# Kernel tuning notes

Measured on AMD Instinct MI355X. Metric: run time of the kernel, lower is better.

Reference implementation:

```python
import jax, jax.numpy as jnp
import numpy as np

N = 50000      # nodes
E = 800000     # directed edges (avg degree 16)
F_IN = 128     # in_channels
HID = 256      # hidden_channels
OUT = 40       # out_channels (classes)


def setup_inputs() -> dict:
    key = jax.random.key(0)
    ks = jax.random.split(key, 6)
    x = jax.random.normal(ks[0], (N, F_IN), dtype=jnp.float32)
    edge_index = jax.random.randint(ks[1], (2, E), 0, N, dtype=jnp.int32)
    W1 = jax.random.normal(ks[2], (F_IN, HID), dtype=jnp.float32) * (1.0 / np.sqrt(F_IN))
    b1 = jnp.zeros((HID,), jnp.float32)
    W2 = jax.random.normal(ks[3], (HID, HID), dtype=jnp.float32) * (1.0 / np.sqrt(HID))
    b2 = jnp.zeros((HID,), jnp.float32)
    Wc = jax.random.normal(ks[4], (HID, OUT), dtype=jnp.float32) * (1.0 / np.sqrt(HID))
    bc = jnp.zeros((OUT,), jnp.float32)
    return {"x": x, "W1": W1, "b1": b1, "W2": W2, "b2": b2,
            "Wc": Wc, "bc": bc, "edge_index": edge_index}


def _gcn_conv(x, W, b, src, dst, norm):
    # PyG GCNConv: linear transform, then normalized sparse aggregation, then bias.
    h = x @ W                                    # [N, H]
    msg = h[src] * norm[:, None]                 # [E+N, H] gather + scale
    agg = jax.ops.segment_sum(msg, dst, num_segments=N)  # scatter-add
    return agg + b


def reference(x, W1, b1, W2, b2, Wc, bc, edge_index):
    # add self-loops (GCNConv default add_self_loops=True)
    loops = jnp.arange(N, dtype=edge_index.dtype)
    src = jnp.concatenate([edge_index[0], loops])
    dst = jnp.concatenate([edge_index[1], loops])
    # symmetric normalization D^-1/2 A D^-1/2 (degree counted at dst)
    deg = jax.ops.segment_sum(jnp.ones_like(dst, dtype=jnp.float32), dst,
                              num_segments=N)
    dinv = jax.lax.rsqrt(jnp.maximum(deg, 1.0))  # deg >= 1 due to self-loops
    norm = dinv[src] * dinv[dst]                 # [E+N]
    # layer 1 + ReLU (dropout is identity in eval mode)
    h = jax.nn.relu(_gcn_conv(x, W1, b1, src, dst, norm))
    # layer 2 + ReLU
    h = jax.nn.relu(_gcn_conv(h, W2, b2, src, dst, norm))
    # dense classifier
    return h @ Wc + bc  # [N, OUT]
```

## Files before the change

### kernel.cpp

```cpp
#include <hip/hip_runtime.h>

#define NNODES 50000
#define NEDGES 800000
#define F_IN   128
#define HID    256
#define NOUT   40
#define NBLK_SCAN ((NNODES + 255) / 256)
#define NBLK_CAST 6250
#define NBLK_DEG  2048
#define NBLK_PREP 432
#define EDGE_CHUNK 3125
#define NODES_PER_G 6250

typedef __attribute__((ext_vector_type(8))) _Float16 f16x8;
typedef __attribute__((ext_vector_type(4))) float f32x4;
typedef __attribute__((ext_vector_type(4))) unsigned short u16x4;
typedef __attribute__((ext_vector_type(8))) unsigned short u16x8;

__device__ __forceinline__ unsigned short f2h(float f) {
  return __builtin_bit_cast(unsigned short, (_Float16)f);
}
__device__ __forceinline__ float h2f(unsigned short u) {
  return (float)__builtin_bit_cast(_Float16, u);
}


__global__ __launch_bounds__(256) void k_pre(const float* __restrict__ X,
                                             unsigned short* __restrict__ Xh,
                                             const int* __restrict__ dst,
                                             int* __restrict__ count,
                                             const float* __restrict__ W1,
                                             const float* __restrict__ W2,
                                             const float* __restrict__ Wc,
                                             unsigned short* __restrict__ T1,
                                             unsigned short* __restrict__ T2,
                                             unsigned short* __restrict__ Tc) {
  int b = blockIdx.x, t = threadIdx.x;
  if (b < NBLK_CAST) {
    int i = b * 256 + t;
    float4 v = *reinterpret_cast<const float4*>(X + (size_t)i * 4);
    ushort4 o;
    o.x = f2h(v.x); o.y = f2h(v.y); o.z = f2h(v.z); o.w = f2h(v.w);
    *reinterpret_cast<ushort4*>(Xh + (size_t)i * 4) = o;
  } else if (b < NBLK_CAST + NBLK_DEG) {
    int db = b - NBLK_CAST;
    int g = b & 7;
    int chunk = db >> 3;
    int lo = g * NODES_PER_G, hi = lo + NODES_PER_G;
    int base = chunk * EDGE_CHUNK;
    for (int i = base + t; i < base + EDGE_CHUNK; i += 256) {
      int d = dst[i];
      if (d >= lo && d < hi) atomicAdd(&count[d], 1);
    }
  } else {
    int pb = b - NBLK_CAST - NBLK_DEG;
    if (pb < 128) {
      int idx = pb * 256 + t;
      int n = idx >> 7, k = idx & 127;
      T1[idx] = f2h(W1[(size_t)k * HID + n]);
    } else if (pb < 384) {
      int idx = (pb - 128) * 256 + t;
      int n = idx >> 8, k = idx & 255;
      T2[idx] = f2h(W2[(size_t)k * HID + n]);
    } else {
      int idx = (pb - 384) * 256 + t;
      int n = idx >> 8, k = idx & 255;
      float v = (n < NOUT) ? Wc[(size_t)k * NOUT + n] : 0.f;
      Tc[idx] = f2h(v);
    }
  }
}


__global__ __launch_bounds__(256) void k_scan1(const int* __restrict__ count,
                                               int* __restrict__ rowstart,
                                               int* __restrict__ bsum,
                                               float* __restrict__ dinv) {
  __shared__ int tmp[256];
  int t = threadIdx.x;
  int i = blockIdx.x * 256 + t;
  int v = (i < NNODES) ? count[i] : 0;
  if (i < NNODES) dinv[i] = rsqrtf((float)(v + 1));
  tmp[t] = v;
  __syncthreads();
  for (int off = 1; off < 256; off <<= 1) {
    int x = (t >= off) ? tmp[t - off] : 0;
    __syncthreads();
    tmp[t] += x;
    __syncthreads();
  }
  if (i < NNODES) rowstart[i] = tmp[t] - v;
  if (t == 255) bsum[blockIdx.x] = tmp[255];
}

__global__ __launch_bounds__(256) void k_scan2(const int* __restrict__ bsum,
                                               int* __restrict__ boff) {
  __shared__ int tmp[256];
  int t = threadIdx.x;
  int v = (t < NBLK_SCAN) ? bsum[t] : 0;
  tmp[t] = v;
  __syncthreads();
  for (int off = 1; off < 256; off <<= 1) {
    int x = (t >= off) ? tmp[t - off] : 0;
    __syncthreads();
    tmp[t] += x;
    __syncthreads();
  }
  if (t < NBLK_SCAN) boff[t] = tmp[t] - v;
}


__global__ __launch_bounds__(256) void k_scatter(const int* __restrict__ src,
                                                 const int* __restrict__ dst,
                                                 const int* __restrict__ rowstart,
                                                 const int* __restrict__ boff,
                                                 int* __restrict__ cursor,
                                                 int* __restrict__ csr) {
  int g = blockIdx.x & 7;
  int chunk = blockIdx.x >> 3;
  int lo = g * NODES_PER_G, hi = lo + NODES_PER_G;
  int base = chunk * EDGE_CHUNK;
  for (int i = base + threadIdx.x; i < base + EDGE_CHUNK; i += 256) {
    int d = dst[i];
    if (d >= lo && d < hi) {
      int p = rowstart[d] + boff[d >> 8] + atomicAdd(&cursor[d], 1);
      csr[p] = src[i];
    }
  }
}


__global__ __launch_bounds__(256) void k_agg1(const unsigned short* __restrict__ X,
                                              const int* __restrict__ rowstart,
                                              const int* __restrict__ boff,
                                              const int* __restrict__ csr,
                                              const float* __restrict__ dinv,
                                              uint2* __restrict__ Y) {
  int wave = threadIdx.x >> 6, lane = threadIdx.x & 63;
  int node = blockIdx.x * 4 + wave;
  if (node >= NNODES) return;
  int half = lane >> 5, l32 = lane & 31;
  float di = dinv[node];
  float a[4] = {0.f, 0.f, 0.f, 0.f};
  int e = rowstart[node] + boff[node >> 8];
  int end = (node + 1 < NNODES) ? rowstart[node + 1] + boff[(node + 1) >> 8] : NEDGES;
  for (; e + 8 <= end; e += 8) {
    int s0 = csr[e + 0 + half], s1 = csr[e + 2 + half];
    int s2 = csr[e + 4 + half], s3 = csr[e + 6 + half];
    float w0 = dinv[s0] * di, w1 = dinv[s1] * di;
    float w2 = dinv[s2] * di, w3 = dinv[s3] * di;
    u16x4 r0 = *reinterpret_cast<const u16x4*>(X + (size_t)s0 * F_IN + l32 * 4);
    u16x4 r1 = *reinterpret_cast<const u16x4*>(X + (size_t)s1 * F_IN + l32 * 4);
    u16x4 r2 = *reinterpret_cast<const u16x4*>(X + (size_t)s2 * F_IN + l32 * 4);
    u16x4 r3 = *reinterpret_cast<const u16x4*>(X + (size_t)s3 * F_IN + l32 * 4);
#pragma unroll
    for (int k = 0; k < 4; k++) {
      a[k] = fmaf(h2f(r0[k]), w0, a[k]);
      a[k] = fmaf(h2f(r1[k]), w1, a[k]);
      a[k] = fmaf(h2f(r2[k]), w2, a[k]);
      a[k] = fmaf(h2f(r3[k]), w3, a[k]);
    }
  }
  for (; e + 2 <= end; e += 2) {
    int s = csr[e + half];
    float w = dinv[s] * di;
    u16x4 r = *reinterpret_cast<const u16x4*>(X + (size_t)s * F_IN + l32 * 4);
#pragma unroll
    for (int k = 0; k < 4; k++) a[k] = fmaf(h2f(r[k]), w, a[k]);
  }
  if (e < end) {
    int s = csr[e];
    float w = half ? 0.f : dinv[s] * di;
    u16x4 r = *reinterpret_cast<const u16x4*>(X + (size_t)s * F_IN + l32 * 4);
#pragma unroll
    for (int k = 0; k < 4; k++) a[k] = fmaf(h2f(r[k]), w, a[k]);
  }
#pragma unroll
  for (int k = 0; k < 4; k++) a[k] += __shfl_xor(a[k], 32);
  if (half == 0) {
    u16x4 self = *reinterpret_cast<const u16x4*>(X + (size_t)node * F_IN + l32 * 4);
    float dd = di * di;
#pragma unroll
    for (int k = 0; k < 4; k++) a[k] = fmaf(h2f(self[k]), dd, a[k]);
    uint2 o;
    o.x = (unsigned)f2h(a[0]) | ((unsigned)f2h(a[1]) << 16);
    o.y = (unsigned)f2h(a[2]) | ((unsigned)f2h(a[3]) << 16);
    Y[(size_t)node * 32 + l32] = o;
  }
}


__global__ __launch_bounds__(256) void k_agg2(const unsigned short* __restrict__ H,
                                              const int* __restrict__ rowstart,
                                              const int* __restrict__ boff,
                                              const int* __restrict__ csr,
                                              const float* __restrict__ dinv,
                                              uint4* __restrict__ Y) {
  int wave = threadIdx.x >> 6, lane = threadIdx.x & 63;
  int node = blockIdx.x * 4 + wave;
  if (node >= NNODES) return;
  int half = lane >> 5, l32 = lane & 31;
  float di = dinv[node];
  float a[8] = {0.f, 0.f, 0.f, 0.f, 0.f, 0.f, 0.f, 0.f};
  int e = rowstart[node] + boff[node >> 8];
  int end = (node + 1 < NNODES) ? rowstart[node + 1] + boff[(node + 1) >> 8] : NEDGES;
  for (; e + 8 <= end; e += 8) {
    int s0 = csr[e + 0 + half], s1 = csr[e + 2 + half];
    int s2 = csr[e + 4 + half], s3 = csr[e + 6 + half];
    float w0 = dinv[s0] * di, w1 = dinv[s1] * di;
    float w2 = dinv[s2] * di, w3 = dinv[s3] * di;
    u16x8 r0 = *reinterpret_cast<const u16x8*>(H + (size_t)s0 * HID + l32 * 8);
    u16x8 r1 = *reinterpret_cast<const u16x8*>(H + (size_t)s1 * HID + l32 * 8);
    u16x8 r2 = *reinterpret_cast<const u16x8*>(H + (size_t)s2 * HID + l32 * 8);
    u16x8 r3 = *reinterpret_cast<const u16x8*>(H + (size_t)s3 * HID + l32 * 8);
#pragma unroll
    for (int k = 0; k < 8; k++) {
      a[k] = fmaf(h2f(r0[k]), w0, a[k]);
      a[k] = fmaf(h2f(r1[k]), w1, a[k]);
      a[k] = fmaf(h2f(r2[k]), w2, a[k]);
      a[k] = fmaf(h2f(r3[k]), w3, a[k]);
    }
  }
  for (; e + 2 <= end; e += 2) {
    int s = csr[e + half];
    float w = dinv[s] * di;
    u16x8 r = *reinterpret_cast<const u16x8*>(H + (size_t)s * HID + l32 * 8);
#pragma unroll
    for (int k = 0; k < 8; k++) a[k] = fmaf(h2f(r[k]), w, a[k]);
  }
  if (e < end) {
    int s = csr[e];
    float w = half ? 0.f : dinv[s] * di;
    u16x8 r = *reinterpret_cast<const u16x8*>(H + (size_t)s * HID + l32 * 8);
#pragma unroll
    for (int k = 0; k < 8; k++) a[k] = fmaf(h2f(r[k]), w, a[k]);
  }
#pragma unroll
  for (int k = 0; k < 8; k++) a[k] += __shfl_xor(a[k], 32);
  if (half == 0) {
    u16x8 self = *reinterpret_cast<const u16x8*>(H + (size_t)node * HID + l32 * 8);
    float dd = di * di;
#pragma unroll
    for (int k = 0; k < 8; k++) a[k] = fmaf(h2f(self[k]), dd, a[k]);
    uint4 o;
    o.x = (unsigned)f2h(a[0]) | ((unsigned)f2h(a[1]) << 16);
    o.y = (unsigned)f2h(a[2]) | ((unsigned)f2h(a[3]) << 16);
    o.z = (unsigned)f2h(a[4]) | ((unsigned)f2h(a[5]) << 16);
    o.w = (unsigned)f2h(a[6]) | ((unsigned)f2h(a[7]) << 16);
    Y[(size_t)node * 32 + l32] = o;
  }
}


template <int RELU, int OMODE>
__global__ __launch_bounds__(256) void k_mgemm(const unsigned short* __restrict__ Ag,
                                               const unsigned short* __restrict__ Btg,
                                               const float* __restrict__ bias,
                                               void* __restrict__ Cout,
                                               int M, int Nc, int K) {
  __shared__ unsigned short Ah[2][128 * 40];
  __shared__ unsigned short Bh[2][128 * 40];
  int tid = threadIdx.x;
  int lane = tid & 63, w = tid >> 6;
  int wr = w >> 1, wc = w & 1;
  int bm = blockIdx.x * 128, bn = blockIdx.y * 128;
  int l15 = lane & 15, kg = lane >> 4;
  int row0 = tid >> 2, kq0 = (tid & 3) * 8;
  int gm0 = bm + row0, gm1 = bm + row0 + 64;

  f32x4 zero = {0.f, 0.f, 0.f, 0.f};
  f32x4 acc[4][4];
#pragma unroll
  for (int i = 0; i < 4; i++)
#pragma unroll
    for (int j = 0; j < 4; j++) acc[i][j] = zero;

  uint4 ra0, ra1, rb0, rb1;
  const uint4 z4 = {0, 0, 0, 0};
#define LOADT(KT)                                                                    \
  {                                                                                  \
    ra0 = z4; ra1 = z4;                                                              \
    if (gm0 < M) ra0 = *reinterpret_cast<const uint4*>(Ag + (size_t)gm0 * K + (KT) + kq0); \
    if (gm1 < M) ra1 = *reinterpret_cast<const uint4*>(Ag + (size_t)gm1 * K + (KT) + kq0); \
    rb0 = *reinterpret_cast<const uint4*>(Btg + (size_t)(bn + row0) * K + (KT) + kq0);     \
    rb1 = *reinterpret_cast<const uint4*>(Btg + (size_t)(bn + row0 + 64) * K + (KT) + kq0);\
  }
#define STORET(B)                                                       \
  {                                                                     \
    *reinterpret_cast<uint4*>(&Ah[B][row0 * 40 + kq0]) = ra0;           \
    *reinterpret_cast<uint4*>(&Ah[B][(row0 + 64) * 40 + kq0]) = ra1;    \
    *reinterpret_cast<uint4*>(&Bh[B][row0 * 40 + kq0]) = rb0;           \
    *reinterpret_cast<uint4*>(&Bh[B][(row0 + 64) * 40 + kq0]) = rb1;    \
  }

  LOADT(0);
  STORET(0);
  __syncthreads();
  int nt = K >> 5, cur = 0;
  for (int t = 0; t < nt; t++) {
    bool pf = (t + 1 < nt);
    if (pf) LOADT((t + 1) << 5);
    f16x8 fa[4], fb[4];
#pragma unroll
    for (int f = 0; f < 4; f++) {
      fa[f] = *reinterpret_cast<const f16x8*>(&Ah[cur][(wr * 64 + f * 16 + l15) * 40 + kg * 8]);
      fb[f] = *reinterpret_cast<const f16x8*>(&Bh[cur][(wc * 64 + f * 16 + l15) * 40 + kg * 8]);
    }
#pragma unroll
    for (int i = 0; i < 4; i++)
#pragma unroll
      for (int j = 0; j < 4; j++)
        acc[i][j] = __builtin_amdgcn_mfma_f32_16x16x32_f16(fa[i], fb[j], acc[i][j], 0, 0, 0);
    if (pf) STORET(cur ^ 1);
    __syncthreads();
    cur ^= 1;
  }
#undef LOADT
#undef STORET

  int r0 = kg * 4;
#pragma unroll
  for (int i = 0; i < 4; i++) {
    int gmBase = bm + wr * 64 + i * 16 + r0;
#pragma unroll
    for (int r = 0; r < 4; r++) {
      int gm = gmBase + r;
      if (gm >= M) continue;
#pragma unroll
      for (int j = 0; j < 4; j++) {
        int gn = bn + wc * 64 + j * 16 + l15;
        if (gn >= Nc) continue;
        float v = acc[i][j][r] + bias[gn];
        if (RELU) v = fmaxf(v, 0.f);
        size_t o = (size_t)gm * Nc + gn;
        if (OMODE == 0) ((float*)Cout)[o] = v;
        else            ((unsigned short*)Cout)[o] = f2h(v);
      }
    }
  }
}


__global__ __launch_bounds__(256) void k_cls(const unsigned short* __restrict__ Ag,
                                             const unsigned short* __restrict__ Btg,
                                             const float* __restrict__ bias,
                                             float* __restrict__ C, int M) {
  __shared__ unsigned short As[256 * 40];
  __shared__ unsigned short Bs[48 * 40];
  int tid = threadIdx.x;
  int lane = tid & 63, w = tid >> 6;
  int l15 = lane & 15, kg = lane >> 4;
  int bm = blockIdx.x * 256;

  f32x4 zero = {0.f, 0.f, 0.f, 0.f};
  f32x4 acc[4][3];
#pragma unroll
  for (int i = 0; i < 4; i++)
#pragma unroll
    for (int j = 0; j < 3; j++) acc[i][j] = zero;

  for (int kt = 0; kt < HID; kt += 32) {
#pragma unroll
    for (int it = 0; it < 4; it++) {
      int c = tid + it * 256;
      int row = c >> 2, kq = (c & 3) * 8;
      int gm = bm + row;
      uint4 v = {0, 0, 0, 0};
      if (gm < M) v = *reinterpret_cast<const uint4*>(Ag + (size_t)gm * HID + kt + kq);
      *reinterpret_cast<uint4*>(&As[row * 40 + kq]) = v;
    }
    if (tid < 192) {
      int row = tid >> 2, kq = (tid & 3) * 8;
      *reinterpret_cast<uint4*>(&Bs[row * 40 + kq]) =
          *reinterpret_cast<const uint4*>(Btg + (size_t)row * HID + kt + kq);
    }
    __syncthreads();
    f16x8 fa[4], fb[3];
#pragma unroll
    for (int f = 0; f < 4; f++)
      fa[f] = *reinterpret_cast<const f16x8*>(&As[(w * 64 + f * 16 + l15) * 40 + kg * 8]);
#pragma unroll
    for (int j = 0; j < 3; j++)
      fb[j] = *reinterpret_cast<const f16x8*>(&Bs[(j * 16 + l15) * 40 + kg * 8]);
#pragma unroll
    for (int i = 0; i < 4; i++)
#pragma unroll
      for (int j = 0; j < 3; j++)
        acc[i][j] = __builtin_amdgcn_mfma_f32_16x16x32_f16(fa[i], fb[j], acc[i][j], 0, 0, 0);
    __syncthreads();
  }

  int r0 = kg * 4;
#pragma unroll
  for (int i = 0; i < 4; i++) {
    int gmBase = bm + w * 64 + i * 16 + r0;
#pragma unroll
    for (int r = 0; r < 4; r++) {
      int gm = gmBase + r;
      if (gm >= M) continue;
#pragma unroll
      for (int j = 0; j < 3; j++) {
        int gn = j * 16 + l15;
        if (gn >= NOUT) continue;
        C[(size_t)gm * NOUT + gn] = acc[i][j][r] + bias[gn];
      }
    }
  }
}


extern "C" void kernel_launch(void* const* d_in, const int* in_sizes, int n_in,
                              void* d_out, int out_size, void* d_ws, size_t ws_size,
                              hipStream_t stream) {
  (void)in_sizes; (void)n_in; (void)out_size; (void)ws_size;
  const float* x  = (const float*)d_in[0];
  const float* W1 = (const float*)d_in[1];
  const float* b1 = (const float*)d_in[2];
  const float* W2 = (const float*)d_in[3];
  const float* b2 = (const float*)d_in[4];
  const float* Wc = (const float*)d_in[5];
  const float* bc = (const float*)d_in[6];
  const int* edge = (const int*)d_in[7];
  const int* srcE = edge;
  const int* dstE = edge + NEDGES;
  float* out = (float*)d_out;

  char* ws = (char*)d_ws;
  int*   count    = (int*)(ws + 0);
  int*   cursor   = (int*)(ws + 200064);
  int*   rowstart = (int*)(ws + 400128);
  float* dinv     = (float*)(ws + 600320);
  int*   csr      = (int*)(ws + 800384);
  int*   bsum     = (int*)(ws + 4000512);
  int*   boff     = (int*)(ws + 4001536);
  unsigned short* W1t = (unsigned short*)(ws + 4002560);
  unsigned short* W2t = (unsigned short*)(ws + 4068096);
  unsigned short* Wct = (unsigned short*)(ws + 4199168);
  unsigned short* xh  = (unsigned short*)(ws + 4264704);
  unsigned short* aggx = (unsigned short*)(ws + 17064704);
  unsigned short* h1   = (unsigned short*)(ws + 29864704);
  unsigned short* aggh = (unsigned short*)(ws + 55464704);
  unsigned short* h2   = (unsigned short*)(ws + 81064704);

  hipMemsetAsync(ws, 0, 400128, stream);

  k_pre<<<NBLK_CAST + NBLK_DEG + NBLK_PREP, 256, 0, stream>>>(
      x, xh, dstE, count, W1, W2, Wc, W1t, W2t, Wct);
  k_scan1<<<NBLK_SCAN, 256, 0, stream>>>(count, rowstart, bsum, dinv);
  k_scan2<<<1, 256, 0, stream>>>(bsum, boff);
  k_scatter<<<NBLK_DEG, 256, 0, stream>>>(srcE, dstE, rowstart, boff, cursor, csr);

  k_agg1<<<(NNODES + 3) / 4, 256, 0, stream>>>(xh, rowstart, boff, csr, dinv, (uint2*)aggx);
  {
    dim3 grid((NNODES + 127) / 128, HID / 128);
    k_mgemm<1, 1><<<grid, 256, 0, stream>>>(aggx, W1t, b1, (void*)h1, NNODES, HID, F_IN);
  }
  k_agg2<<<(NNODES + 3) / 4, 256, 0, stream>>>(h1, rowstart, boff, csr, dinv, (uint4*)aggh);
  {
    dim3 grid((NNODES + 127) / 128, HID / 128);
    k_mgemm<1, 1><<<grid, 256, 0, stream>>>(aggh, W2t, b2, (void*)h2, NNODES, HID, HID);
  }
  k_cls<<<(NNODES + 255) / 256, 256, 0, stream>>>(h2, Wct, bc, out, NNODES);
}
```

Measured before the change: 343.3 us.

## Slice features into 32-column slabs for cache-resident gather aggregation

Feature matrices (xh, aggx, h1, aggh, h2) are stored as column slabs of 32 halves per node, and the aggregation kernels are rewritten so each block handles one slab for a chunk of nodes. Each wave processes 8 nodes, with 8 lanes per edge and 8 edges in flight. The idea is that one slab (about 3.2MB) fits in L2/MALL, so random neighbor gathers hit cache instead of DRAM. The GEMM and classifier kernels are adapted to read and write the slab layout. The cost is that csr and dinv are re-read once per slice, and the GEMM's strided slab loads may be less contiguous.

```diff
diff --git a/kernel.cpp b/kernel.cpp
--- a/kernel.cpp
+++ b/kernel.cpp
@@ -11,11 +11,10 @@
 #define NBLK_PREP 432
 #define EDGE_CHUNK 3125
 #define NODES_PER_G 6250
+#define NCHUNK_AGG 1563
 
 typedef __attribute__((ext_vector_type(8))) _Float16 f16x8;
 typedef __attribute__((ext_vector_type(4))) float f32x4;
-typedef __attribute__((ext_vector_type(4))) unsigned short u16x4;
-typedef __attribute__((ext_vector_type(8))) unsigned short u16x8;
 
 __device__ __forceinline__ unsigned short f2h(float f) {
   return __builtin_bit_cast(unsigned short, (_Float16)f);
@@ -38,10 +37,13 @@
   int b = blockIdx.x, t = threadIdx.x;
   if (b < NBLK_CAST) {
     int i = b * 256 + t;
+    int node = i >> 5, c = i & 31;
+    int slab = c >> 3, off = (c & 7) * 4;
     float4 v = *reinterpret_cast<const float4*>(X + (size_t)i * 4);
     ushort4 o;
     o.x = f2h(v.x); o.y = f2h(v.y); o.z = f2h(v.z); o.w = f2h(v.w);
-    *reinterpret_cast<ushort4*>(Xh + (size_t)i * 4) = o;
+    *reinterpret_cast<ushort4*>(Xh + (size_t)slab * (NNODES * 32) +
+                                (size_t)node * 32 + off) = o;
   } else if (b < NBLK_CAST + NBLK_DEG) {
     int db = b - NBLK_CAST;
     int g = b & 7;
@@ -130,129 +132,87 @@
 }
 
 
-__global__ __launch_bounds__(256) void k_agg1(const unsigned short* __restrict__ X,
+template <int NSLICE>
+__global__ __launch_bounds__(256) void k_aggs(const unsigned short* __restrict__ X,
                                               const int* __restrict__ rowstart,
                                               const int* __restrict__ boff,
                                               const int* __restrict__ csr,
                                               const float* __restrict__ dinv,
-                                              uint2* __restrict__ Y) {
+                                              unsigned short* __restrict__ Y) {
+  constexpr int SSH = (NSLICE == 8) ? 3 : 2;
+  int slice = blockIdx.x & (NSLICE - 1);
+  int chunk = blockIdx.x >> SSH;
+  const unsigned short* Xs = X + (size_t)slice * (NNODES * 32);
+  unsigned short* Ys = Y + (size_t)slice * (NNODES * 32);
   int wave = threadIdx.x >> 6, lane = threadIdx.x & 63;
-  int node = blockIdx.x * 4 + wave;
-  if (node >= NNODES) return;
-  int half = lane >> 5, l32 = lane & 31;
-  float di = dinv[node];
-  float a[4] = {0.f, 0.f, 0.f, 0.f};
-  int e = rowstart[node] + boff[node >> 8];
-  int end = (node + 1 < NNODES) ? rowstart[node + 1] + boff[(node + 1) >> 8] : NEDGES;
-  for (; e + 8 <= end; e += 8) {
-    int s0 = csr[e + 0 + half], s1 = csr[e + 2 + half];
-    int s2 = csr[e + 4 + half], s3 = csr[e + 6 + half];
-    float w0 = dinv[s0] * di, w1 = dinv[s1] * di;
-    float w2 = dinv[s2] * di, w3 = dinv[s3] * di;
-    u16x4 r0 = *reinterpret_cast<const u16x4*>(X + (size_t)s0 * F_IN + l32 * 4);
-    u16x4 r1 = *reinterpret_cast<const u16x4*>(X + (size_t)s1 * F_IN + l32 * 4);
-    u16x4 r2 = *reinterpret_cast<const u16x4*>(X + (size_t)s2 * F_IN + l32 * 4);
-    u16x4 r3 = *reinterpret_cast<const u16x4*>(X + (size_t)s3 * F_IN + l32 * 4);
-#pragma unroll
-    for (int k = 0; k < 4; k++) {
-      a[k] = fmaf(h2f(r0[k]), w0, a[k]);
-      a[k] = fmaf(h2f(r1[k]), w1, a[k]);
-      a[k] = fmaf(h2f(r2[k]), w2, a[k]);
-      a[k] = fmaf(h2f(r3[k]), w3, a[k]);
-    }
-  }
-  for (; e + 2 <= end; e += 2) {
-    int s = csr[e + half];
-    float w = dinv[s] * di;
-    u16x4 r = *reinterpret_cast<const u16x4*>(X + (size_t)s * F_IN + l32 * 4);
-#pragma unroll
-    for (int k = 0; k < 4; k++) a[k] = fmaf(h2f(r[k]), w, a[k]);
-  }
-  if (e < end) {
-    int s = csr[e];
-    float w = half ? 0.f : dinv[s] * di;
-    u16x4 r = *reinterpret_cast<const u16x4*>(X + (size_t)s * F_IN + l32 * 4);
-#pragma unroll
-    for (int k = 0; k < 4; k++) a[k] = fmaf(h2f(r[k]), w, a[k]);
-  }
-#pragma unroll
-  for (int k = 0; k < 4; k++) a[k] += __shfl_xor(a[k], 32);
-  if (half == 0) {
-    u16x4 self = *reinterpret_cast<const u16x4*>(X + (size_t)node * F_IN + l32 * 4);
-    float dd = di * di;
-#pragma unroll
-    for (int k = 0; k < 4; k++) a[k] = fmaf(h2f(self[k]), dd, a[k]);
-    uint2 o;
-    o.x = (unsigned)f2h(a[0]) | ((unsigned)f2h(a[1]) << 16);
-    o.y = (unsigned)f2h(a[2]) | ((unsigned)f2h(a[3]) << 16);
-    Y[(size_t)node * 32 + l32] = o;
-  }
-}
-
-
-__global__ __launch_bounds__(256) void k_agg2(const unsigned short* __restrict__ H,
-                                              const int* __restrict__ rowstart,
-                                              const int* __restrict__ boff,
-                                              const int* __restrict__ csr,
-                                              const float* __restrict__ dinv,
-                                              uint4* __restrict__ Y) {
-  int wave = threadIdx.x >> 6, lane = threadIdx.x & 63;
-  int node = blockIdx.x * 4 + wave;
-  if (node >= NNODES) return;
-  int half = lane >> 5, l32 = lane & 31;
-  float di = dinv[node];
-  float a[8] = {0.f, 0.f, 0.f, 0.f, 0.f, 0.f, 0.f, 0.f};
-  int e = rowstart[node] + boff[node >> 8];
-  int end = (node + 1 < NNODES) ? rowstart[node + 1] + boff[(node + 1) >> 8] : NEDGES;
-  for (; e + 8 <= end; e += 8) {
-    int s0 = csr[e + 0 + half], s1 = csr[e + 2 + half];
-    int s2 = csr[e + 4 + half], s3 = csr[e + 6 + half];
-    float w0 = dinv[s0] * di, w1 = dinv[s1] * di;
-    float w2 = dinv[s2] * di, w3 = dinv[s3] * di;
-    u16x8 r0 = *reinterpret_cast<const u16x8*>(H + (size_t)s0 * HID + l32 * 8);
-    u16x8 r1 = *reinterpret_cast<const u16x8*>(H + (size_t)s1 * HID + l32 * 8);
-    u16x8 r2 = *reinterpret_cast<const u16x8*>(H + (size_t)s2 * HID + l32 * 8);
-    u16x8 r3 = *reinterpret_cast<const u16x8*>(H + (size_t)s3 * HID + l32 * 8);
-#pragma unroll
-    for (int k = 0; k < 8; k++) {
-      a[k] = fmaf(h2f(r0[k]), w0, a[k]);
-      a[k] = fmaf(h2f(r1[k]), w1, a[k]);
-      a[k] = fmaf(h2f(r2[k]), w2, a[k]);
-      a[k] = fmaf(h2f(r3[k]), w3, a[k]);
-    }
-  }
-  for (; e + 2 <= end; e += 2) {
-    int s = csr[e + half];
-    float w = dinv[s] * di;
-    u16x8 r = *reinterpret_cast<const u16x8*>(H + (size_t)s * HID + l32 * 8);
-#pragma unroll
-    for (int k = 0; k < 8; k++) a[k] = fmaf(h2f(r[k]), w, a[k]);
-  }
-  if (e < end) {
-    int s = csr[e];
-    float w = half ? 0.f : dinv[s] * di;
-    u16x8 r = *reinterpret_cast<const u16x8*>(H + (size_t)s * HID + l32 * 8);
-#pragma unroll
-    for (int k = 0; k < 8; k++) a[k] = fmaf(h2f(r[k]), w, a[k]);
-  }
-#pragma unroll
-  for (int k = 0; k < 8; k++) a[k] += __shfl_xor(a[k], 32);
-  if (half == 0) {
-    u16x8 self = *reinterpret_cast<const u16x8*>(H + (size_t)node * HID + l32 * 8);
-    float dd = di * di;
-#pragma unroll
-    for (int k = 0; k < 8; k++) a[k] = fmaf(h2f(self[k]), dd, a[k]);
-    uint4 o;
-    o.x = (unsigned)f2h(a[0]) | ((unsigned)f2h(a[1]) << 16);
-    o.y = (unsigned)f2h(a[2]) | ((unsigned)f2h(a[3]) << 16);
-    o.z = (unsigned)f2h(a[4]) | ((unsigned)f2h(a[5]) << 16);
-    o.w = (unsigned)f2h(a[6]) | ((unsigned)f2h(a[7]) << 16);
-    Y[(size_t)node * 32 + l32] = o;
-  }
-}
-
-
-template <int RELU, int OMODE>
+  int grp = lane >> 3, l8 = lane & 7;
+  int n0 = (chunk * 4 + wave) * 8;
+  for (int ni = 0; ni < 8; ni++) {
+    int node = n0 + ni;
+    if (node >= NNODES) return;
+    float di = dinv[node];
+    int e = rowstart[node] + boff[node >> 8];
+    int end = (node + 1 < NNODES) ? rowstart[node + 1] + boff[(node + 1) >> 8] : NEDGES;
+    float a0 = 0.f, a1 = 0.f, a2 = 0.f, a3 = 0.f;
+    for (; e + 16 <= end; e += 16) {
+      int sA = __builtin_nontemporal_load(&csr[e + grp]);
+      int sB = __builtin_nontemporal_load(&csr[e + 8 + grp]);
+      float wA = dinv[sA] * di, wB = dinv[sB] * di;
+      uint2 vA = *reinterpret_cast<const uint2*>(Xs + (size_t)sA * 32 + l8 * 4);
+      uint2 vB = *reinterpret_cast<const uint2*>(Xs + (size_t)sB * 32 + l8 * 4);
+      a0 = fmaf(h2f((unsigned short)vA.x), wA, a0);
+      a1 = fmaf(h2f((unsigned short)(vA.x >> 16)), wA, a1);
+      a2 = fmaf(h2f((unsigned short)vA.y), wA, a2);
+      a3 = fmaf(h2f((unsigned short)(vA.y >> 16)), wA, a3);
+      a0 = fmaf(h2f((unsigned short)vB.x), wB, a0);
+      a1 = fmaf(h2f((unsigned short)(vB.x >> 16)), wB, a1);
+      a2 = fmaf(h2f((unsigned short)vB.y), wB, a2);
+      a3 = fmaf(h2f((unsigned short)(vB.y >> 16)), wB, a3);
+    }
+    for (; e + 8 <= end; e += 8) {
+      int s = __builtin_nontemporal_load(&csr[e + grp]);
+      float w = dinv[s] * di;
+      uint2 v = *reinterpret_cast<const uint2*>(Xs + (size_t)s * 32 + l8 * 4);
+      a0 = fmaf(h2f((unsigned short)v.x), w, a0);
+      a1 = fmaf(h2f((unsigned short)(v.x >> 16)), w, a1);
+      a2 = fmaf(h2f((unsigned short)v.y), w, a2);
+      a3 = fmaf(h2f((unsigned short)(v.y >> 16)), w, a3);
+    }
+    int rem = end - e;
+    if (rem > 0) {
+      int s = __builtin_nontemporal_load(&csr[e + (grp < rem ? grp : 0)]);
+      float w = (grp < rem) ? dinv[s] * di : 0.f;
+      uint2 v = *reinterpret_cast<const uint2*>(Xs + (size_t)s * 32 + l8 * 4);
+      a0 = fmaf(h2f((unsigned short)v.x), w, a0);
+      a1 = fmaf(h2f((unsigned short)(v.x >> 16)), w, a1);
+      a2 = fmaf(h2f((unsigned short)v.y), w, a2);
+      a3 = fmaf(h2f((unsigned short)(v.y >> 16)), w, a3);
+    }
+#pragma unroll
+    for (int off = 8; off < 64; off <<= 1) {
+      a0 += __shfl_xor(a0, off);
+      a1 += __shfl_xor(a1, off);
+      a2 += __shfl_xor(a2, off);
+      a3 += __shfl_xor(a3, off);
+    }
+    if (grp == 0) {
+      uint2 v = *reinterpret_cast<const uint2*>(Xs + (size_t)node * 32 + l8 * 4);
+      float dd = di * di;
+      a0 = fmaf(h2f((unsigned short)v.x), dd, a0);
+      a1 = fmaf(h2f((unsigned short)(v.x >> 16)), dd, a1);
+      a2 = fmaf(h2f((unsigned short)v.y), dd, a2);
+      a3 = fmaf(h2f((unsigned short)(v.y >> 16)), dd, a3);
+      unsigned long long o =
+          (unsigned long long)((unsigned)f2h(a0) | ((unsigned)f2h(a1) << 16)) |
+          ((unsigned long long)((unsigned)f2h(a2) | ((unsigned)f2h(a3) << 16)) << 32);
+      __builtin_nontemporal_store(o, reinterpret_cast<unsigned long long*>(
+          Ys + (size_t)node * 32 + l8 * 4));
+    }
+  }
+}
+
+
+template <int RELU, int OMODE, int ALAYOUT>
 __global__ __launch_bounds__(256) void k_mgemm(const unsigned short* __restrict__ Ag,
                                                const unsigned short* __restrict__ Btg,
                                                const float* __restrict__ bias,
@@ -277,12 +237,16 @@
 
   uint4 ra0, ra1, rb0, rb1;
   const uint4 z4 = {0, 0, 0, 0};
-#define LOADT(KT)                                                                    \
-  {                                                                                  \
-    ra0 = z4; ra1 = z4;                                                              \
-    if (gm0 < M) ra0 = *reinterpret_cast<const uint4*>(Ag + (size_t)gm0 * K + (KT) + kq0); \
-    if (gm1 < M) ra1 = *reinterpret_cast<const uint4*>(Ag + (size_t)gm1 * K + (KT) + kq0); \
-    rb0 = *reinterpret_cast<const uint4*>(Btg + (size_t)(bn + row0) * K + (KT) + kq0);     \
+#define LOADT(KT)                                                                     \
+  {                                                                                   \
+    const unsigned short* Ab = ALAYOUT                                                \
+        ? Ag + (size_t)((KT) >> 5) * ((size_t)M * 32) + kq0                           \
+        : Ag + (size_t)(KT) + kq0;                                                    \
+    const size_t astr = ALAYOUT ? 32 : (size_t)K;                                     \
+    ra0 = z4; ra1 = z4;                                                               \
+    if (gm0 < M) ra0 = *reinterpret_cast<const uint4*>(Ab + (size_t)gm0 * astr);      \
+    if (gm1 < M) ra1 = *reinterpret_cast<const uint4*>(Ab + (size_t)gm1 * astr);      \
+    rb0 = *reinterpret_cast<const uint4*>(Btg + (size_t)(bn + row0) * K + (KT) + kq0);\
     rb1 = *reinterpret_cast<const uint4*>(Btg + (size_t)(bn + row0 + 64) * K + (KT) + kq0);\
   }
 #define STORET(B)                                                       \
@@ -332,9 +296,12 @@
         if (gn >= Nc) continue;
         float v = acc[i][j][r] + bias[gn];
         if (RELU) v = fmaxf(v, 0.f);
-        size_t o = (size_t)gm * Nc + gn;
-        if (OMODE == 0) ((float*)Cout)[o] = v;
-        else            ((unsigned short*)Cout)[o] = f2h(v);
+        if (OMODE == 0) {
+          ((float*)Cout)[(size_t)gm * Nc + gn] = v;
+        } else {
+          size_t o = (size_t)(gn >> 5) * ((size_t)M * 32) + (size_t)gm * 32 + (gn & 31);
+          ((unsigned short*)Cout)[o] = f2h(v);
+        }
       }
     }
   }
@@ -360,13 +327,14 @@
     for (int j = 0; j < 3; j++) acc[i][j] = zero;
 
   for (int kt = 0; kt < HID; kt += 32) {
+    const unsigned short* Ab = Ag + (size_t)(kt >> 5) * ((size_t)M * 32);
 #pragma unroll
     for (int it = 0; it < 4; it++) {
       int c = tid + it * 256;
       int row = c >> 2, kq = (c & 3) * 8;
       int gm = bm + row;
       uint4 v = {0, 0, 0, 0};
-      if (gm < M) v = *reinterpret_cast<const uint4*>(Ag + (size_t)gm * HID + kt + kq);
+      if (gm < M) v = *reinterpret_cast<const uint4*>(Ab + (size_t)gm * 32 + kq);
       *reinterpret_cast<uint4*>(&As[row * 40 + kq]) = v;
     }
     if (tid < 192) {
@@ -450,15 +418,15 @@
   k_scan2<<<1, 256, 0, stream>>>(bsum, boff);
   k_scatter<<<NBLK_DEG, 256, 0, stream>>>(srcE, dstE, rowstart, boff, cursor, csr);
 
-  k_agg1<<<(NNODES + 3) / 4, 256, 0, stream>>>(xh, rowstart, boff, csr, dinv, (uint2*)aggx);
+  k_aggs<4><<<NCHUNK_AGG << 2, 256, 0, stream>>>(xh, rowstart, boff, csr, dinv, aggx);
   {
     dim3 grid((NNODES + 127) / 128, HID / 128);
-    k_mgemm<1, 1><<<grid, 256, 0, stream>>>(aggx, W1t, b1, (void*)h1, NNODES, HID, F_IN);
-  }
-  k_agg2<<<(NNODES + 3) / 4, 256, 0, stream>>>(h1, rowstart, boff, csr, dinv, (uint4*)aggh);
+    k_mgemm<1, 1, 1><<<grid, 256, 0, stream>>>(aggx, W1t, b1, (void*)h1, NNODES, HID, F_IN);
+  }
+  k_aggs<8><<<NCHUNK_AGG << 3, 256, 0, stream>>>(h1, rowstart, boff, csr, dinv, aggh);
   {
     dim3 grid((NNODES + 127) / 128, HID / 128);
-    k_mgemm<1, 1><<<grid, 256, 0, stream>>>(aggh, W2t, b2, (void*)h2, NNODES, HID, HID);
+    k_mgemm<1, 1, 1><<<grid, 256, 0, stream>>>(aggh, W2t, b2, (void*)h2, NNODES, HID, HID);
   }
   k_cls<<<(NNODES + 255) / 256, 256, 0, stream>>>(h2, Wct, bc, out, NNODES);
 }
```

Result: slower. 515.7 us (+50.2%).

## Fuse layer-2 GEMM with classifier and merge scan kernels via last-block pattern

Applied to the files above, without the earlier changes.

The layer-2 GEMM and the classifier GEMM are fused into one kernel. Each block computes a 128-row slab of h2 in two 128-column halves, keeps the ReLU output in shared memory, and feeds it straight into the classifier MFMAs, so h2 is never written to or read back from global memory. The second scan kernel is folded into the first using an atomic done-counter, so the last block to finish computes the block offsets, which removes one launch. In exchange the fused kernel launches only about 391 blocks instead of 782, uses more shared memory, and drops the double-buffered global-to-LDS pipeline, which may lower occupancy and latency hiding.

```diff
diff --git a/kernel.cpp b/kernel.cpp
--- a/kernel.cpp
+++ b/kernel.cpp
@@ -75,8 +75,11 @@
 __global__ __launch_bounds__(256) void k_scan1(const int* __restrict__ count,
                                                int* __restrict__ rowstart,
                                                int* __restrict__ bsum,
-                                               float* __restrict__ dinv) {
+                                               float* __restrict__ dinv,
+                                               int* __restrict__ boff,
+                                               int* __restrict__ done) {
   __shared__ int tmp[256];
+  __shared__ int lastFlag;
   int t = threadIdx.x;
   int i = blockIdx.x * 256 + t;
   int v = (i < NNODES) ? count[i] : 0;
@@ -90,23 +93,26 @@
     __syncthreads();
   }
   if (i < NNODES) rowstart[i] = tmp[t] - v;
-  if (t == 255) bsum[blockIdx.x] = tmp[255];
-}
-
-__global__ __launch_bounds__(256) void k_scan2(const int* __restrict__ bsum,
-                                               int* __restrict__ boff) {
-  __shared__ int tmp[256];
-  int t = threadIdx.x;
-  int v = (t < NBLK_SCAN) ? bsum[t] : 0;
-  tmp[t] = v;
+  if (t == 255) {
+    bsum[blockIdx.x] = tmp[255];
+    __threadfence();
+  }
   __syncthreads();
-  for (int off = 1; off < 256; off <<= 1) {
-    int x = (t >= off) ? tmp[t - off] : 0;
+  if (t == 0) lastFlag = (atomicAdd(done, 1) == (int)gridDim.x - 1);
+  __syncthreads();
+  if (lastFlag) {
+    __threadfence();
+    int v2 = (t < NBLK_SCAN) ? bsum[t] : 0;
+    tmp[t] = v2;
     __syncthreads();
-    tmp[t] += x;
-    __syncthreads();
-  }
-  if (t < NBLK_SCAN) boff[t] = tmp[t] - v;
+    for (int off = 1; off < 256; off <<= 1) {
+      int x2 = (t >= off) ? tmp[t - off] : 0;
+      __syncthreads();
+      tmp[t] += x2;
+      __syncthreads();
+    }
+    if (t < NBLK_SCAN) boff[t] = tmp[t] - v2;
+  }
 }
 
 
@@ -252,11 +258,10 @@
 }
 
 
-template <int RELU, int OMODE>
 __global__ __launch_bounds__(256) void k_mgemm(const unsigned short* __restrict__ Ag,
                                                const unsigned short* __restrict__ Btg,
                                                const float* __restrict__ bias,
-                                               void* __restrict__ Cout,
+                                               unsigned short* __restrict__ Cout,
                                                int M, int Nc, int K) {
   __shared__ unsigned short Ah[2][128 * 40];
   __shared__ unsigned short Bh[2][128 * 40];
@@ -329,71 +334,111 @@
 #pragma unroll
       for (int j = 0; j < 4; j++) {
         int gn = bn + wc * 64 + j * 16 + l15;
-        if (gn >= Nc) continue;
         float v = acc[i][j][r] + bias[gn];
-        if (RELU) v = fmaxf(v, 0.f);
-        size_t o = (size_t)gm * Nc + gn;
-        if (OMODE == 0) ((float*)Cout)[o] = v;
-        else            ((unsigned short*)Cout)[o] = f2h(v);
+        v = fmaxf(v, 0.f);
+        Cout[(size_t)gm * Nc + gn] = f2h(v);
       }
     }
   }
 }
 
 
-__global__ __launch_bounds__(256) void k_cls(const unsigned short* __restrict__ Ag,
-                                             const unsigned short* __restrict__ Btg,
-                                             const float* __restrict__ bias,
-                                             float* __restrict__ C, int M) {
-  __shared__ unsigned short As[256 * 40];
-  __shared__ unsigned short Bs[48 * 40];
+__global__ __launch_bounds__(256) void k_g2cls(const unsigned short* __restrict__ Ag,
+                                               const unsigned short* __restrict__ W2t,
+                                               const float* __restrict__ b2,
+                                               const unsigned short* __restrict__ Wct,
+                                               const float* __restrict__ bc,
+                                               float* __restrict__ out, int M) {
+  __shared__ unsigned short Ah[128 * 40];
+  __shared__ unsigned short Bh[128 * 40];
+  __shared__ unsigned short H2[128 * 136];
+  __shared__ unsigned short WcS[48 * 40];
   int tid = threadIdx.x;
   int lane = tid & 63, w = tid >> 6;
+  int wr = w >> 1, wc = w & 1;
+  int bm = blockIdx.x * 128;
   int l15 = lane & 15, kg = lane >> 4;
-  int bm = blockIdx.x * 256;
+  int row0 = tid >> 2, kq0 = (tid & 3) * 8;
+  int gm0 = bm + row0, gm1 = bm + row0 + 64;
 
   f32x4 zero = {0.f, 0.f, 0.f, 0.f};
-  f32x4 acc[4][3];
-#pragma unroll
-  for (int i = 0; i < 4; i++)
-#pragma unroll
-    for (int j = 0; j < 3; j++) acc[i][j] = zero;
-
-  for (int kt = 0; kt < HID; kt += 32) {
-#pragma unroll
-    for (int it = 0; it < 4; it++) {
-      int c = tid + it * 256;
-      int row = c >> 2, kq = (c & 3) * 8;
-      int gm = bm + row;
-      uint4 v = {0, 0, 0, 0};
-      if (gm < M) v = *reinterpret_cast<const uint4*>(Ag + (size_t)gm * HID + kt + kq);
-      *reinterpret_cast<uint4*>(&As[row * 40 + kq]) = v;
-    }
-    if (tid < 192) {
-      int row = tid >> 2, kq = (tid & 3) * 8;
-      *reinterpret_cast<uint4*>(&Bs[row * 40 + kq]) =
-          *reinterpret_cast<const uint4*>(Btg + (size_t)row * HID + kt + kq);
-    }
+  f32x4 clsacc[2][3];
+#pragma unroll
+  for (int f = 0; f < 2; f++)
+#pragma unroll
+    for (int j = 0; j < 3; j++) clsacc[f][j] = zero;
+
+  for (int halfN = 0; halfN < 2; halfN++) {
+    f32x4 acc[4][4];
+#pragma unroll
+    for (int i = 0; i < 4; i++)
+#pragma unroll
+      for (int j = 0; j < 4; j++) acc[i][j] = zero;
+    int bn = halfN * 128;
+    for (int kt = 0; kt < HID; kt += 32) {
+      uint4 ra0 = {0, 0, 0, 0}, ra1 = {0, 0, 0, 0};
+      if (gm0 < M) ra0 = *reinterpret_cast<const uint4*>(Ag + (size_t)gm0 * HID + kt + kq0);
+      if (gm1 < M) ra1 = *reinterpret_cast<const uint4*>(Ag + (size_t)gm1 * HID + kt + kq0);
+      uint4 rb0 = *reinterpret_cast<const uint4*>(W2t + (size_t)(bn + row0) * HID + kt + kq0);
+      uint4 rb1 = *reinterpret_cast<const uint4*>(W2t + (size_t)(bn + row0 + 64) * HID + kt + kq0);
+      *reinterpret_cast<uint4*>(&Ah[row0 * 40 + kq0]) = ra0;
+      *reinterpret_cast<uint4*>(&Ah[(row0 + 64) * 40 + kq0]) = ra1;
+      *reinterpret_cast<uint4*>(&Bh[row0 * 40 + kq0]) = rb0;
+      *reinterpret_cast<uint4*>(&Bh[(row0 + 64) * 40 + kq0]) = rb1;
+      __syncthreads();
+      f16x8 fa[4], fb[4];
+#pragma unroll
+      for (int f = 0; f < 4; f++) {
+        fa[f] = *reinterpret_cast<const f16x8*>(&Ah[(wr * 64 + f * 16 + l15) * 40 + kg * 8]);
+        fb[f] = *reinterpret_cast<const f16x8*>(&Bh[(wc * 64 + f * 16 + l15) * 40 + kg * 8]);
+      }
+#pragma unroll
+      for (int i = 0; i < 4; i++)
+#pragma unroll
+        for (int j = 0; j < 4; j++)
+          acc[i][j] = __builtin_amdgcn_mfma_f32_16x16x32_f16(fa[i], fb[j], acc[i][j], 0, 0, 0);
+      __syncthreads();
+    }
+    int r0 = kg * 4;
+#pragma unroll
+    for (int i = 0; i < 4; i++)
+#pragma unroll
+      for (int r = 0; r < 4; r++) {
+        int lrow = wr * 64 + i * 16 + r0 + r;
+#pragma unroll
+        for (int j = 0; j < 4; j++) {
+          int lcol = wc * 64 + j * 16 + l15;
+          float v = acc[i][j][r] + b2[bn + lcol];
+          H2[lrow * 136 + lcol] = f2h(fmaxf(v, 0.f));
+        }
+      }
     __syncthreads();
-    f16x8 fa[4], fb[3];
-#pragma unroll
-    for (int f = 0; f < 4; f++)
-      fa[f] = *reinterpret_cast<const f16x8*>(&As[(w * 64 + f * 16 + l15) * 40 + kg * 8]);
-#pragma unroll
-    for (int j = 0; j < 3; j++)
-      fb[j] = *reinterpret_cast<const f16x8*>(&Bs[(j * 16 + l15) * 40 + kg * 8]);
-#pragma unroll
-    for (int i = 0; i < 4; i++)
+    for (int kt2 = 0; kt2 < 128; kt2 += 32) {
+      if (tid < 192) {
+        int row = tid >> 2, kq = (tid & 3) * 8;
+        *reinterpret_cast<uint4*>(&WcS[row * 40 + kq]) =
+            *reinterpret_cast<const uint4*>(Wct + (size_t)row * HID + halfN * 128 + kt2 + kq);
+      }
+      __syncthreads();
+      f16x8 fa[2], fb[3];
+#pragma unroll
+      for (int f = 0; f < 2; f++)
+        fa[f] = *reinterpret_cast<const f16x8*>(&H2[(w * 32 + f * 16 + l15) * 136 + kt2 + kg * 8]);
 #pragma unroll
       for (int j = 0; j < 3; j++)
-        acc[i][j] = __builtin_amdgcn_mfma_f32_16x16x32_f16(fa[i], fb[j], acc[i][j], 0, 0, 0);
-    __syncthreads();
-  }
-
+        fb[j] = *reinterpret_cast<const f16x8*>(&WcS[(j * 16 + l15) * 40 + kg * 8]);
+#pragma unroll
+      for (int f = 0; f < 2; f++)
+#pragma unroll
+        for (int j = 0; j < 3; j++)
+          clsacc[f][j] = __builtin_amdgcn_mfma_f32_16x16x32_f16(fa[f], fb[j], clsacc[f][j], 0, 0, 0);
+      __syncthreads();
+    }
+  }
   int r0 = kg * 4;
 #pragma unroll
-  for (int i = 0; i < 4; i++) {
-    int gmBase = bm + w * 64 + i * 16 + r0;
+  for (int f = 0; f < 2; f++) {
+    int gmBase = bm + w * 32 + f * 16 + r0;
 #pragma unroll
     for (int r = 0; r < 4; r++) {
       int gm = gmBase + r;
@@ -402,7 +447,7 @@
       for (int j = 0; j < 3; j++) {
         int gn = j * 16 + l15;
         if (gn >= NOUT) continue;
-        C[(size_t)gm * NOUT + gn] = acc[i][j][r] + bias[gn];
+        out[(size_t)gm * NOUT + gn] = clsacc[f][j][r] + bc[gn];
       }
     }
   }
@@ -428,6 +473,7 @@
   char* ws = (char*)d_ws;
   int*   count    = (int*)(ws + 0);
   int*   cursor   = (int*)(ws + 200064);
+  int*   done     = (int*)(ws + 400064);
   int*   rowstart = (int*)(ws + 400128);
   float* dinv     = (float*)(ws + 600320);
   int*   csr      = (int*)(ws + 800384);
@@ -440,25 +486,19 @@
   unsigned short* aggx = (unsigned short*)(ws + 17064704);
   unsigned short* h1   = (unsigned short*)(ws + 29864704);
   unsigned short* aggh = (unsigned short*)(ws + 55464704);
-  unsigned short* h2   = (unsigned short*)(ws + 81064704);
 
   hipMemsetAsync(ws, 0, 400128, stream);
 
   k_pre<<<NBLK_CAST + NBLK_DEG + NBLK_PREP, 256, 0, stream>>>(
       x, xh, dstE, count, W1, W2, Wc, W1t, W2t, Wct);
-  k_scan1<<<NBLK_SCAN, 256, 0, stream>>>(count, rowstart, bsum, dinv);
-  k_scan2<<<1, 256, 0, stream>>>(bsum, boff);
+  k_scan1<<<NBLK_SCAN, 256, 0, stream>>>(count, rowstart, bsum, dinv, boff, done);
   k_scatter<<<NBLK_DEG, 256, 0, stream>>>(srcE, dstE, rowstart, boff, cursor, csr);
 
   k_agg1<<<(NNODES + 3) / 4, 256, 0, stream>>>(xh, rowstart, boff, csr, dinv, (uint2*)aggx);
   {
     dim3 grid((NNODES + 127) / 128, HID / 128);
-    k_mgemm<1, 1><<<grid, 256, 0, stream>>>(aggx, W1t, b1, (void*)h1, NNODES, HID, F_IN);
+    k_mgemm<<<grid, 256, 0, stream>>>(aggx, W1t, b1, h1, NNODES, HID, F_IN);
   }
   k_agg2<<<(NNODES + 3) / 4, 256, 0, stream>>>(h1, rowstart, boff, csr, dinv, (uint4*)aggh);
-  {
-    dim3 grid((NNODES + 127) / 128, HID / 128);
-    k_mgemm<1, 1><<<grid, 256, 0, stream>>>(aggh, W2t, b2, (void*)h2, NNODES, HID, HID);
-  }
-  k_cls<<<(NNODES + 255) / 256, 256, 0, stream>>>(h2, Wct, bc, out, NNODES);
-}
+  k_g2cls<<<(NNODES + 127) / 128, 256, 0, stream>>>(aggh, W2t, b2, Wct, bc, out, NNODES);
+}
```

After: 308.7 us. -10.1%, faster.
